# Kernel optimization log

Measured on AMD Instinct MI355X. Metric: run time of the kernel, lower is better.

Reference implementation:

```python
import jax, jax.numpy as jnp
import numpy as np

L, B, S, D = 8, 1, 4096, 2048
H, KVH, HD = 16, 2, 128
Q = 32
THETA = 1e6
MROPE = (16, 24, 24)  # mrope_section, sums to HD//2
EPS = 1e-6


def setup_inputs() -> dict:
    key = jax.random.key(0)
    ks = jax.random.split(key, 8)
    hidden_states = jax.random.normal(ks[0], (L, B, S, D), dtype=jnp.float32)
    ln_w = jax.random.uniform(ks[1], (L, D), dtype=jnp.float32, minval=0.5, maxval=1.5)
    q_w = jax.random.normal(ks[2], (L, D, H * HD), dtype=jnp.float32) * 0.02
    q_b = jax.random.normal(ks[3], (L, H * HD), dtype=jnp.float32) * 0.02
    k_w = jax.random.normal(ks[4], (L, D, KVH * HD), dtype=jnp.float32) * 0.02
    k_b = jax.random.normal(ks[5], (L, KVH * HD), dtype=jnp.float32) * 0.02
    position_ids = jax.random.randint(ks[6], (3, B, S), 0, S, dtype=jnp.int32)
    q_idx = jnp.sort(jax.random.randint(ks[7], (Q,), 0, S, dtype=jnp.int32))
    return {"hidden_states": hidden_states, "ln_w": ln_w, "q_w": q_w, "q_b": q_b,
            "k_w": k_w, "k_b": k_b, "position_ids": position_ids, "q_idx": q_idx}


def _rot_half(x):
    h = x.shape[-1] // 2
    return jnp.concatenate([-x[..., h:], x[..., :h]], axis=-1)


def _mrope_combine(t):
    # t: (3, B, S, HD). Split last dim per 2*mrope_section, chunk i taken from axis i%3.
    parts, off = [], 0
    for i, sec in enumerate(MROPE):
        w = 2 * sec
        parts.append(t[i % 3, :, :, off:off + w])
        off += w
    return jnp.concatenate(parts, axis=-1)[:, None, :, :]  # (B, 1, S, HD)


def reference(hidden_states, ln_w, q_w, q_b, k_w, k_b, position_ids, q_idx):
    # Rotary embeddings from 3D mRoPE position ids
    inv_freq = 1.0 / (THETA ** (jnp.arange(0, HD, 2, dtype=jnp.float32) / HD))  # (HD/2,)
    freqs = position_ids.astype(jnp.float32)[..., None] * inv_freq  # (3, B, S, HD/2)
    emb = jnp.concatenate([freqs, freqs], axis=-1)  # (3, B, S, HD)
    cos = _mrope_combine(jnp.cos(emb))  # (B, 1, S, HD)
    sin = _mrope_combine(jnp.sin(emb))
    cos_q = cos[:, :, q_idx, :]  # (B, 1, Q, HD)
    sin_q = sin[:, :, q_idx, :]
    # Eager causal mask sliced at query rows: (Q, S)
    mask_add = jnp.where(jnp.arange(S)[None, :] > q_idx[:, None], -1e9, 0.0).astype(jnp.float32)

    scale = 1.0 / np.sqrt(HD).astype(np.float32)

    def per_layer(hs, lw, qw, qb, kw, kb):
        # RMSNorm (input_layernorm)
        var = jnp.mean(jnp.square(hs), axis=-1, keepdims=True)
        x = hs * jax.lax.rsqrt(var + EPS) * lw  # (B, S, D)
        xq = x[:, q_idx, :]  # (B, Q, D)
        k = (jnp.einsum('bsd,de->bse', x, kw) + kb).reshape(B, S, KVH, HD).transpose(0, 2, 1, 3)
        q = (jnp.einsum('bqd,de->bqe', xq, qw) + qb).reshape(B, Q, H, HD).transpose(0, 2, 1, 3)
        k = jnp.repeat(k, H // KVH, axis=1)  # repeat_kv -> (B, H, S, HD)
        k = k * cos + _rot_half(k) * sin
        q = q * cos_q + _rot_half(q) * sin_q
        scores = jnp.einsum('bhqd,bhkd->bhqk', q, k) * scale  # (B, H, Q, S)
        scores = scores + mask_add[None, None]
        return jax.nn.softmax(scores.astype(jnp.float32), axis=-1)

    return jax.vmap(per_layer)(hidden_states, ln_w, q_w, q_b, k_w, k_b)  # (L, B, H, Q, S)
```

## Files before the change

kernel.cpp:

```cpp
#include <hip/hip_runtime.h>
#include <hip/hip_bf16.h>
#include <math.h>

#define LYR 8
#define SEQ 4096
#define DIM 2048
#define NH 16
#define HD 128
#define NQ 32
#define NKV 256
#define NQE 2048

typedef __attribute__((ext_vector_type(8))) short short8;
typedef __attribute__((ext_vector_type(4))) float f32x4;

#define WS_IRQ   0
#define WS_ABLOB 256
#define WS_COS   524544
#define WS_SIN   1048832
#define WS_QBUF  1573120
#define WS_PART  2097408
#define WS_W2    4194560
#define WS_KBLOB 8388864
#define WS_QBLOB 16777472

__device__ __forceinline__ short f2bf(float x) {
  __hip_bfloat16 h = __float2bfloat16(x);
  return *(short*)&h;
}
__device__ __forceinline__ float bf2f(short s) {
  unsigned u = ((unsigned)(unsigned short)s) << 16;
  return __uint_as_float(u);
}

#define GLOAD16(srcp, dstp) \
  __builtin_amdgcn_global_load_lds( \
      (const __attribute__((address_space(1))) unsigned int*)(srcp), \
      (__attribute__((address_space(3))) unsigned int*)(dstp), 16, 0, 0)

__global__ __launch_bounds__(256) void prep_kernel(
    const float* __restrict__ ln_w, const float* __restrict__ k_w,
    short* __restrict__ W2) {
  int kb = blockIdx.x, l = blockIdx.y, t = threadIdx.x;
  const float* kwl = k_w + (size_t)l * DIM * NKV;
  const float* lnl = ln_w + l * DIM;
  short* blob = W2 + (size_t)(l * 64 + kb) * 16384;
  #pragma unroll
  for (int i = 0; i < 4; ++i) {
    int p = t + i * 256;
    int fi = p >> 6, lane = p & 63;
    int n = fi * 16 + (lane & 15);
    int k0 = kb * 32 + (lane >> 4) * 8;
    short hi8[8], lo8[8];
    #pragma unroll
    for (int e = 0; e < 8; ++e) {
      float v = lnl[k0 + e] * kwl[(size_t)(k0 + e) * NKV + n];
      short h = f2bf(v);
      hi8[e] = h;
      lo8[e] = f2bf(v - bf2f(h));
    }
    *(short8*)(blob + p * 8) = *(short8*)hi8;
    *(short8*)(blob + 8192 + p * 8) = *(short8*)lo8;
  }
}

__global__ __launch_bounds__(256) void rmsq_kernel(const float* __restrict__ hs,
                                                   const int* __restrict__ q_idx,
                                                   float* __restrict__ irq) {
  int qi = blockIdx.x, l = blockIdx.y, t = threadIdx.x;
  int s = q_idx[qi];
  const float* row = hs + ((size_t)l * SEQ + s) * DIM;
  float4 v0 = *(const float4*)(row + t * 4);
  float4 v1 = *(const float4*)(row + t * 4 + 1024);
  float acc = v0.x*v0.x + v0.y*v0.y + v0.z*v0.z + v0.w*v0.w
            + v1.x*v1.x + v1.y*v1.y + v1.z*v1.z + v1.w*v1.w;
  #pragma unroll
  for (int off = 32; off >= 1; off >>= 1) acc += __shfl_down(acc, off);
  __shared__ float red[4];
  if ((t & 63) == 0) red[t >> 6] = acc;
  __syncthreads();
  if (t == 0) {
    float tot = red[0] + red[1] + red[2] + red[3];
    irq[l * NQ + qi] = rsqrtf(tot / (float)DIM + 1e-6f);
  }
}

__global__ void cossin_kernel(const int* __restrict__ pos_ids,
                              float* __restrict__ cost, float* __restrict__ sint) {
  int idx = blockIdx.x * 256 + threadIdx.x;
  int s = idx >> 7, d = idx & 127;
  int t = (d < 32) ? 0 : (d < 80 ? 1 : 2);
  int j = d & 63;
  double invf = pow(1000000.0, -(double)j / 64.0);
  double ph = (double)pos_ids[t * SEQ + s] * invf;
  cost[idx] = (float)cos(ph);
  sint[idx] = (float)sin(ph);
}

__global__ __launch_bounds__(256) void xqt_kernel(
    const float* __restrict__ hs, const float* __restrict__ ln_w,
    const int* __restrict__ q_idx, const float* __restrict__ irq,
    short* __restrict__ Ablob) {
  __shared__ int qix[32];
  __shared__ float qir[32];
  int l = blockIdx.x, t = threadIdx.x;
  if (t < 32) { qix[t] = q_idx[t]; qir[t] = irq[l * NQ + t]; }
  __syncthreads();
  int lane = t & 63, g4 = t >> 6;
  short* base = Ablob + (size_t)l * 131072;
  int row = lane & 15, kgl = lane >> 4;
  for (int i = 0; i < 64; ++i) {
    int group = g4 * 64 + i;
    int kb = group >> 2, half = (group >> 1) & 1, mf = group & 1;
    int r = row + mf * 16;
    int k0 = kb * 32 + kgl * 8;
    const float* src = hs + ((size_t)l * SEQ + qix[r]) * DIM + k0;
    const float* lnp = ln_w + l * DIM + k0;
    float ir = qir[r];
    float4 v0 = *(const float4*)src;
    float4 v1 = *(const float4*)(src + 4);
    float4 w0 = *(const float4*)lnp;
    float4 w1 = *(const float4*)(lnp + 4);
    float av[8] = {v0.x*w0.x, v0.y*w0.y, v0.z*w0.z, v0.w*w0.w,
                   v1.x*w1.x, v1.y*w1.y, v1.z*w1.z, v1.w*w1.w};
    short o8[8];
    #pragma unroll
    for (int e = 0; e < 8; ++e) {
      float v = av[e] * ir;
      short h = f2bf(v);
      o8[e] = half ? f2bf(v - bf2f(h)) : h;
    }
    *(short8*)(base + group * 512 + lane * 8) = *(short8*)o8;
  }
}

__global__ __launch_bounds__(256) void kgemm_kernel(
    const float* __restrict__ hs, const short* __restrict__ W2,
    const float* __restrict__ k_b, const float* __restrict__ cost,
    const float* __restrict__ sint, short* __restrict__ Kblob) {
  __shared__ __align__(1024) char SM[81920];

  int t = threadIdx.x;
  int fid = blockIdx.x;
  int l = fid & 7, sb = fid >> 3;
  int s0 = sb * 64;
  int lane = t & 63, w = t >> 6;
  int fr = lane & 15, kg = lane >> 4;
  int arow = t >> 2, akg = t & 3;

  const float* hrow = hs + ((size_t)l * SEQ + s0 + arow) * DIM + akg * 8;
  const char* wbase = (const char*)(W2 + (size_t)l * 64 * 16384);

  int amf = arow >> 4;
  int awoff = amf * 1024 + (((akg * 16 + (arow & 15)) * 16) ^ (akg << 5));
  int aroff = (lane * 16) ^ ((lane >> 4) << 5);

  f32x4 acc[4][4];
  #pragma unroll
  for (int mf = 0; mf < 4; ++mf)
    #pragma unroll
    for (int nf = 0; nf < 4; ++nf) acc[mf][nf] = (f32x4){0.f, 0.f, 0.f, 0.f};
  float sq = 0.f;
  float4 rA0, rA1, rB0, rB1;

  {
    #pragma unroll
    for (int c = 0; c < 8; ++c) {
      int chunk = w * 8 + c;
      GLOAD16(wbase + chunk * 1024 + lane * 16, SM + 16384 + chunk * 1024);
    }
    float4 a0 = *(const float4*)(hrow);
    float4 a1 = *(const float4*)(hrow + 4);
    float av[8] = {a0.x, a0.y, a0.z, a0.w, a1.x, a1.y, a1.z, a1.w};
    short hi8[8], lo8[8];
    #pragma unroll
    for (int e = 0; e < 8; ++e) {
      sq += av[e] * av[e];
      short h = f2bf(av[e]);
      hi8[e] = h;
      lo8[e] = f2bf(av[e] - bf2f(h));
    }
    *(short8*)(SM + awoff) = *(short8*)hi8;
    *(short8*)(SM + 4096 + awoff) = *(short8*)lo8;
    rA0 = *(const float4*)(hrow + 32);
    rA1 = *(const float4*)(hrow + 36);
  }
  __syncthreads();

#define KSTEP(KB, C0, C1, N0, N1) do { \
    int buf_ = (KB) & 1; \
    char* asb_ = SM + buf_ * 8192; \
    char* bsb_ = SM + 16384 + buf_ * 32768; \
    if ((KB) < 63) { \
      const char* src_ = wbase + (size_t)((KB) + 1) * 32768; \
      char* dst_ = SM + 16384 + (buf_ ^ 1) * 32768; \
      _Pragma("unroll") \
      for (int c = 0; c < 8; ++c) { \
        int chunk_ = w * 8 + c; \
        GLOAD16(src_ + chunk_ * 1024 + lane * 16, dst_ + chunk_ * 1024); \
      } \
    } \
    if ((KB) < 62) { \
      N0 = *(const float4*)(hrow + ((KB) + 2) * 32); \
      N1 = *(const float4*)(hrow + ((KB) + 2) * 32 + 4); \
    } \
    short8 ah_[4], al_[4]; \
    _Pragma("unroll") \
    for (int mf = 0; mf < 4; ++mf) { \
      ah_[mf] = *(const short8*)(asb_ + mf * 1024 + aroff); \
      al_[mf] = *(const short8*)(asb_ + 4096 + mf * 1024 + aroff); \
    } \
    __builtin_amdgcn_s_setprio(1); \
    _Pragma("unroll") \
    for (int nf = 0; nf < 4; ++nf) { \
      int f_ = w + nf * 4; \
      short8 bh_ = *(const short8*)(bsb_ + f_ * 1024 + lane * 16); \
      short8 bl_ = *(const short8*)(bsb_ + 16384 + f_ * 1024 + lane * 16); \
      _Pragma("unroll") \
      for (int mf = 0; mf < 4; ++mf) { \
        acc[mf][nf] = __builtin_amdgcn_mfma_f32_16x16x32_bf16(ah_[mf], bh_, acc[mf][nf], 0, 0, 0); \
        acc[mf][nf] = __builtin_amdgcn_mfma_f32_16x16x32_bf16(ah_[mf], bl_, acc[mf][nf], 0, 0, 0); \
        acc[mf][nf] = __builtin_amdgcn_mfma_f32_16x16x32_bf16(al_[mf], bh_, acc[mf][nf], 0, 0, 0); \
      } \
    } \
    __builtin_amdgcn_s_setprio(0); \
    if ((KB) < 63) { \
      char* asn_ = SM + (buf_ ^ 1) * 8192; \
      float av_[8] = {C0.x, C0.y, C0.z, C0.w, C1.x, C1.y, C1.z, C1.w}; \
      short hi8_[8], lo8_[8]; \
      _Pragma("unroll") \
      for (int e = 0; e < 8; ++e) { \
        sq += av_[e] * av_[e]; \
        short h_ = f2bf(av_[e]); \
        hi8_[e] = h_; \
        lo8_[e] = f2bf(av_[e] - bf2f(h_)); \
      } \
      *(short8*)(asn_ + awoff) = *(short8*)hi8_; \
      *(short8*)(asn_ + 4096 + awoff) = *(short8*)lo8_; \
    } \
    __syncthreads(); \
  } while (0)

  for (int kb2 = 0; kb2 < 32; ++kb2) {
    KSTEP(2 * kb2, rA0, rA1, rB0, rB1);
    KSTEP(2 * kb2 + 1, rB0, rB1, rA0, rA1);
  }
#undef KSTEP

  sq += __shfl_xor(sq, 1);
  sq += __shfl_xor(sq, 2);
  float* irs = (float*)(SM + 66560);
  if ((t & 3) == 0) irs[arow] = rsqrtf(sq / (float)DIM + 1e-6f);
  __syncthreads();

  float* Kraw = (float*)SM;
  int j = w * 16 + fr;
  float bias0 = k_b[l * NKV + j];
  float bias1 = k_b[l * NKV + j + 64];
  float bias2 = k_b[l * NKV + j + 128];
  float bias3 = k_b[l * NKV + j + 192];
  #pragma unroll
  for (int mf = 0; mf < 4; ++mf) {
    #pragma unroll
    for (int r = 0; r < 4; ++r) {
      int row = mf * 16 + kg * 4 + r;
      int s = s0 + row;
      float ir = irs[row];
      float v0 = acc[mf][0][r] * ir + bias0;
      float v1 = acc[mf][1][r] * ir + bias1;
      float v2 = acc[mf][2][r] * ir + bias2;
      float v3 = acc[mf][3][r] * ir + bias3;
      float cj = cost[s * HD + j], sj = sint[s * HD + j];
      float cj2 = cost[s * HD + j + 64], sj2 = sint[s * HD + j + 64];
      float* kr = Kraw + row * 260;
      kr[j]       = v0 * cj - v1 * sj;
      kr[j + 64]  = v1 * cj2 + v0 * sj2;
      kr[j + 128] = v2 * cj - v3 * sj;
      kr[j + 192] = v3 * cj2 + v2 * sj2;
    }
  }
  __syncthreads();

  int kc = sb >> 1, fb = (sb & 1) * 4;
  #pragma unroll
  for (int i = 0; i < 8; ++i) {
    int c = t + i * 256;
    int lc = c & 63, fl = (c >> 6) & 3, ts = (c >> 8) & 3, kv = c >> 10;
    int key = fl * 16 + (lc & 15);
    int d0 = kv * 128 + ts * 32 + (lc >> 4) * 8;
    float4 x0 = *(const float4*)(Kraw + key * 260 + d0);
    float4 x1 = *(const float4*)(Kraw + key * 260 + d0 + 4);
    float av[8] = {x0.x, x0.y, x0.z, x0.w, x1.x, x1.y, x1.z, x1.w};
    short hi8[8], lo8[8];
    #pragma unroll
    for (int e = 0; e < 8; ++e) {
      short h = f2bf(av[e]);
      hi8[e] = h;
      lo8[e] = f2bf(av[e] - bf2f(h));
    }
    short* bb = Kblob + (size_t)((l * 2 + kv) * 32 + kc) * 32768
              + (size_t)((ts * 2 + 0) * 8 + fb + fl) * 512 + lc * 8;
    *(short8*)bb = *(short8*)hi8;
    *(short8*)(bb + 4096) = *(short8*)lo8;
  }
}

__global__ __launch_bounds__(512) void qgemm_kernel(
    const float* __restrict__ q_w, const short* __restrict__ Ablob,
    float* __restrict__ part) {
  __shared__ __align__(1024) char SM[131072];
  int t = threadIdx.x;
  int nc = blockIdx.x, ks = blockIdx.y, l = blockIdx.z;
  int lane = t & 63, w = t >> 6;
  int fr = lane & 15, kg = lane >> 4;
  const char* abase = (const char*)(Ablob + (size_t)l * 131072 + (size_t)ks * 32768);
  const float* qwl = q_w + (size_t)l * DIM * NQE;

  #pragma unroll
  for (int c = 0; c < 8; ++c) {
    int chunk = w * 8 + c;
    GLOAD16(abase + chunk * 1024 + lane * 16, SM + chunk * 1024);
  }
  #pragma unroll
  for (int c = 0; c < 4; ++c) {
    int r = w * 4 + c;
    GLOAD16((const char*)(qwl + (size_t)(ks * 512 + r) * NQE + nc * 256) + lane * 16,
            SM + 65536 + r * 1024 + lane * 16);
  }
  f32x4 acc[2][2];
  #pragma unroll
  for (int mf = 0; mf < 2; ++mf)
    #pragma unroll
    for (int nf = 0; nf < 2; ++nf) acc[mf][nf] = (f32x4){0.f, 0.f, 0.f, 0.f};
  __syncthreads();

  for (int ts = 0; ts < 16; ++ts) {
    int buf = ts & 1;
    if (ts < 15) {
      #pragma unroll
      for (int c = 0; c < 4; ++c) {
        int r = w * 4 + c;
        GLOAD16((const char*)(qwl + (size_t)(ks * 512 + (ts + 1) * 32 + r) * NQE + nc * 256) + lane * 16,
                SM + 65536 + (buf ^ 1) * 32768 + r * 1024 + lane * 16);
      }
    }
    short8 ah[2], al[2];
    #pragma unroll
    for (int mf = 0; mf < 2; ++mf) {
      ah[mf] = *(const short8*)(SM + ts * 4096 + mf * 1024 + lane * 16);
      al[mf] = *(const short8*)(SM + ts * 4096 + 2048 + mf * 1024 + lane * 16);
    }
    const float* bt = (const float*)(SM + 65536 + buf * 32768);
    #pragma unroll
    for (int nf = 0; nf < 2; ++nf) {
      int c = w * 32 + nf * 16 + fr;
      short bh8[8], bl8[8];
      #pragma unroll
      for (int e = 0; e < 8; ++e) {
        float v = bt[(kg * 8 + e) * 256 + c];
        short h = f2bf(v);
        bh8[e] = h;
        bl8[e] = f2bf(v - bf2f(h));
      }
      short8 bh = *(short8*)bh8, bl = *(short8*)bl8;
      #pragma unroll
      for (int mf = 0; mf < 2; ++mf) {
        acc[mf][nf] = __builtin_amdgcn_mfma_f32_16x16x32_bf16(ah[mf], bh, acc[mf][nf], 0, 0, 0);
        acc[mf][nf] = __builtin_amdgcn_mfma_f32_16x16x32_bf16(ah[mf], bl, acc[mf][nf], 0, 0, 0);
        acc[mf][nf] = __builtin_amdgcn_mfma_f32_16x16x32_bf16(al[mf], bh, acc[mf][nf], 0, 0, 0);
      }
    }
    __syncthreads();
  }

  #pragma unroll
  for (int mf = 0; mf < 2; ++mf) {
    #pragma unroll
    for (int r = 0; r < 4; ++r) {
      int row = mf * 16 + kg * 4 + r;
      float* prow = part + ((size_t)((ks * LYR + l) * NQ + row)) * NQE + nc * 256;
      #pragma unroll
      for (int nf = 0; nf < 2; ++nf) {
        int col = w * 32 + nf * 16 + fr;
        prow[col] = acc[mf][nf][r];
      }
    }
  }
}

__global__ __launch_bounds__(256) void qred_kernel(
    const float* __restrict__ part, const float* __restrict__ q_b,
    float* __restrict__ Qbuf) {
  int idx = blockIdx.x * 256 + threadIdx.x;
  int n = idx & 2047, q = (idx >> 11) & 31, l = idx >> 16;
  float v = q_b[l * NQE + n];
  #pragma unroll
  for (int ks = 0; ks < 4; ++ks)
    v += part[((size_t)((ks * LYR + l) * NQ + q)) * NQE + n];
  Qbuf[((size_t)l * NQ + q) * NQE + n] = v;
}

__global__ __launch_bounds__(256) void qpack_kernel(
    const float* __restrict__ Qbuf, const float* __restrict__ cost,
    const float* __restrict__ sint, const int* __restrict__ q_idx,
    short* __restrict__ Qblob) {
  int kv = blockIdx.x, l = blockIdx.y, t = threadIdx.x;
  short* blob = Qblob + (size_t)(l * 2 + kv) * 65536;
  #pragma unroll
  for (int i = 0; i < 16; ++i) {
    int p = t + i * 256;
    int ts = p >> 10, f = (p >> 6) & 15, lane = p & 63;
    int row = f * 16 + (lane & 15);
    int hh = row >> 5, q = row & 31;
    int h = kv * 8 + hh;
    int d0 = ts * 32 + (lane >> 4) * 8;
    int s = q_idx[q];
    const float* qrow = Qbuf + ((size_t)l * NQ + q) * NQE + h * HD;
    const float* ct = cost + s * HD;
    const float* st = sint + s * HD;
    short hi8[8], lo8[8];
    #pragma unroll
    for (int e = 0; e < 8; ++e) {
      int d = d0 + e;
      float x = qrow[d];
      float xp = qrow[d ^ 64];
      float v = (d < 64) ? (x * ct[d] - xp * st[d]) : (x * ct[d] + xp * st[d]);
      short h2 = f2bf(v);
      hi8[e] = h2;
      lo8[e] = f2bf(v - bf2f(h2));
    }
    *(short8*)(blob + ((ts * 2 + 0) * 16 + f) * 512 + lane * 8) = *(short8*)hi8;
    *(short8*)(blob + ((ts * 2 + 1) * 16 + f) * 512 + lane * 8) = *(short8*)lo8;
  }
}

__global__ __launch_bounds__(512) void scores_kernel(
    const short* __restrict__ Qblob, const short* __restrict__ Kblob,
    const int* __restrict__ q_idx, float* __restrict__ out) {
  __shared__ short Qs[2][16384];
  __shared__ short Ks[2][8192];
  __shared__ int qiv[32];
  int t = threadIdx.x;
  int kc = blockIdx.x, kv = blockIdx.y, l = blockIdx.z;
  int lane = t & 63, w = t >> 6;
  int wm = w >> 1, wn = w & 1;
  if (t < 32) qiv[t] = q_idx[t];
  const char* qsrc = (const char*)(Qblob + (size_t)(l * 2 + kv) * 65536);
  const char* ksrc = (const char*)(Kblob + (size_t)((l * 2 + kv) * 32 + kc) * 32768);
  #pragma unroll
  for (int c = 0; c < 4; ++c) {
    int off = (w * 4 + c) * 1024;
    GLOAD16(qsrc + off + lane * 16, (char*)Qs[0] + off);
  }
  #pragma unroll
  for (int c = 0; c < 2; ++c) {
    int off = (w * 2 + c) * 1024;
    GLOAD16(ksrc + off + lane * 16, (char*)Ks[0] + off);
  }
  f32x4 acc[4][4];
  #pragma unroll
  for (int mf = 0; mf < 4; ++mf)
    #pragma unroll
    for (int nf = 0; nf < 4; ++nf) acc[mf][nf] = (f32x4){0.f, 0.f, 0.f, 0.f};
  __syncthreads();
  for (int ts = 0; ts < 4; ++ts) {
    int buf = ts & 1;
    if (ts < 3) {
      const char* qs = qsrc + (ts + 1) * 32768;
      const char* ks = ksrc + (ts + 1) * 16384;
      #pragma unroll
      for (int c = 0; c < 4; ++c) {
        int off = (w * 4 + c) * 1024;
        GLOAD16(qs + off + lane * 16, (char*)Qs[(ts + 1) & 1] + off);
      }
      #pragma unroll
      for (int c = 0; c < 2; ++c) {
        int off = (w * 2 + c) * 1024;
        GLOAD16(ks + off + lane * 16, (char*)Ks[(ts + 1) & 1] + off);
      }
    }
    short8 ah[4], al[4];
    #pragma unroll
    for (int mf = 0; mf < 4; ++mf) {
      int f = wm * 4 + mf;
      ah[mf] = *(const short8*)(Qs[buf] + f * 512 + lane * 8);
      al[mf] = *(const short8*)(Qs[buf] + 8192 + f * 512 + lane * 8);
    }
    #pragma unroll
    for (int nf = 0; nf < 4; ++nf) {
      int f = wn * 4 + nf;
      short8 bh = *(const short8*)(Ks[buf] + f * 512 + lane * 8);
      short8 bl = *(const short8*)(Ks[buf] + 4096 + f * 512 + lane * 8);
      #pragma unroll
      for (int mf = 0; mf < 4; ++mf) {
        acc[mf][nf] = __builtin_amdgcn_mfma_f32_16x16x32_bf16(ah[mf], bh, acc[mf][nf], 0, 0, 0);
        acc[mf][nf] = __builtin_amdgcn_mfma_f32_16x16x32_bf16(ah[mf], bl, acc[mf][nf], 0, 0, 0);
        acc[mf][nf] = __builtin_amdgcn_mfma_f32_16x16x32_bf16(al[mf], bh, acc[mf][nf], 0, 0, 0);
      }
    }
    __syncthreads();
  }
  const float scale = 0.088388347648318447f;
  #pragma unroll
  for (int mf = 0; mf < 4; ++mf) {
    #pragma unroll
    for (int r = 0; r < 4; ++r) {
      int rr = wm * 64 + mf * 16 + (lane >> 4) * 4 + r;
      int hh = rr >> 5, q = rr & 31;
      int qv = qiv[q];
      float* orow = out + (((size_t)(l * NH + kv * 8 + hh)) * NQ + q) * SEQ;
      #pragma unroll
      for (int nf = 0; nf < 4; ++nf) {
        int key = kc * 128 + (wn * 4 + nf) * 16 + (lane & 15);
        orow[key] = (key > qv) ? -1e9f : acc[mf][nf][r] * scale;
      }
    }
  }
}

__global__ __launch_bounds__(256) void softmax_kernel(float* __restrict__ out) {
  size_t row = blockIdx.x;
  float* p = out + row * SEQ;
  int t = threadIdx.x;
  float4 v[4];
  float mx = -1e30f;
  #pragma unroll
  for (int i = 0; i < 4; ++i) {
    v[i] = *(const float4*)(p + t * 4 + i * 1024);
    mx = fmaxf(mx, fmaxf(fmaxf(v[i].x, v[i].y), fmaxf(v[i].z, v[i].w)));
  }
  #pragma unroll
  for (int off = 32; off >= 1; off >>= 1) mx = fmaxf(mx, __shfl_xor(mx, off));
  __shared__ float red[4];
  if ((t & 63) == 0) red[t >> 6] = mx;
  __syncthreads();
  mx = fmaxf(fmaxf(red[0], red[1]), fmaxf(red[2], red[3]));
  __syncthreads();
  float sum = 0.f;
  #pragma unroll
  for (int i = 0; i < 4; ++i) {
    v[i].x = __expf(v[i].x - mx); v[i].y = __expf(v[i].y - mx);
    v[i].z = __expf(v[i].z - mx); v[i].w = __expf(v[i].w - mx);
    sum += v[i].x + v[i].y + v[i].z + v[i].w;
  }
  #pragma unroll
  for (int off = 32; off >= 1; off >>= 1) sum += __shfl_xor(sum, off);
  if ((t & 63) == 0) red[t >> 6] = sum;
  __syncthreads();
  sum = red[0] + red[1] + red[2] + red[3];
  float inv = 1.f / sum;
  #pragma unroll
  for (int i = 0; i < 4; ++i) {
    v[i].x *= inv; v[i].y *= inv; v[i].z *= inv; v[i].w *= inv;
    *(float4*)(p + t * 4 + i * 1024) = v[i];
  }
}

extern "C" void kernel_launch(void* const* d_in, const int* in_sizes, int n_in,
                              void* d_out, int out_size, void* d_ws, size_t ws_size,
                              hipStream_t stream) {
  const float* hs   = (const float*)d_in[0];
  const float* ln_w = (const float*)d_in[1];
  const float* q_w  = (const float*)d_in[2];
  const float* q_b  = (const float*)d_in[3];
  const float* k_w  = (const float*)d_in[4];
  const float* k_b  = (const float*)d_in[5];
  const int* pos    = (const int*)d_in[6];
  const int* qidx   = (const int*)d_in[7];
  float* out = (float*)d_out;
  float* ws = (float*)d_ws;
  float* irq   = ws + WS_IRQ;
  short* Ablob = (short*)(ws + WS_ABLOB);
  float* cost  = ws + WS_COS;
  float* sint  = ws + WS_SIN;
  float* Qbuf  = ws + WS_QBUF;
  float* part  = ws + WS_PART;
  short* W2    = (short*)(ws + WS_W2);
  short* Kblob = (short*)(ws + WS_KBLOB);
  short* Qblob = (short*)(ws + WS_QBLOB);

  prep_kernel<<<dim3(64, LYR), 256, 0, stream>>>(ln_w, k_w, W2);
  rmsq_kernel<<<dim3(NQ, LYR), 256, 0, stream>>>(hs, qidx, irq);
  cossin_kernel<<<(SEQ * HD) / 256, 256, 0, stream>>>(pos, cost, sint);
  xqt_kernel<<<LYR, 256, 0, stream>>>(hs, ln_w, qidx, irq, Ablob);
  kgemm_kernel<<<512, 256, 0, stream>>>(hs, W2, k_b, cost, sint, Kblob);
  qgemm_kernel<<<dim3(8, 4, LYR), 512, 0, stream>>>(q_w, Ablob, part);
  qred_kernel<<<2048, 256, 0, stream>>>(part, q_b, Qbuf);
  qpack_kernel<<<dim3(2, LYR), 256, 0, stream>>>(Qbuf, cost, sint, qidx, Qblob);
  scores_kernel<<<dim3(32, 2, LYR), 512, 0, stream>>>(Qblob, Kblob, qidx, out);
  softmax_kernel<<<LYR * NH * NQ, 256, 0, stream>>>(out);
}
```

Before: 277.8 us.

## Load K-GEMM B fragments directly into registers instead of staging through LDS

In the K projection GEMM, each wave now loads its own pre-swizzled weight fragments straight from global memory into double-buffered registers, replacing the global_load_lds staging into shared memory. This cuts the LDS footprint from 80KB to about 65KB and removes the LDS reads for B. The barrier is replaced by a custom one that waits only on lgkmcnt, so outstanding global loads are not drained at each step. The cost is more VGPRs for the register double buffer and direct global-load latency exposed per wave.

```diff
diff --git a/kernel.cpp b/kernel.cpp
--- a/kernel.cpp
+++ b/kernel.cpp
@@ -37,6 +37,8 @@
   __builtin_amdgcn_global_load_lds( \
       (const __attribute__((address_space(1))) unsigned int*)(srcp), \
       (__attribute__((address_space(3))) unsigned int*)(dstp), 16, 0, 0)
+
+#define RBAR() asm volatile("s_waitcnt lgkmcnt(0)\n\ts_barrier" ::: "memory")
 
 __global__ __launch_bounds__(256) void prep_kernel(
     const float* __restrict__ ln_w, const float* __restrict__ k_w,
@@ -138,7 +140,7 @@
     const float* __restrict__ hs, const short* __restrict__ W2,
     const float* __restrict__ k_b, const float* __restrict__ cost,
     const float* __restrict__ sint, short* __restrict__ Kblob) {
-  __shared__ __align__(1024) char SM[81920];
+  __shared__ __align__(1024) char SM[67072];
 
   int t = threadIdx.x;
   int fid = blockIdx.x;
@@ -150,6 +152,7 @@
 
   const float* hrow = hs + ((size_t)l * SEQ + s0 + arow) * DIM + akg * 8;
   const char* wbase = (const char*)(W2 + (size_t)l * 64 * 16384);
+  const char* wfrag = wbase + w * 1024 + lane * 16;
 
   int amf = arow >> 4;
   int awoff = amf * 1024 + (((akg * 16 + (arow & 15)) * 16) ^ (akg << 5));
@@ -162,12 +165,13 @@
     for (int nf = 0; nf < 4; ++nf) acc[mf][nf] = (f32x4){0.f, 0.f, 0.f, 0.f};
   float sq = 0.f;
   float4 rA0, rA1, rB0, rB1;
+  short8 B0h[4], B0l[4], B1h[4], B1l[4];
 
   {
     #pragma unroll
-    for (int c = 0; c < 8; ++c) {
-      int chunk = w * 8 + c;
-      GLOAD16(wbase + chunk * 1024 + lane * 16, SM + 16384 + chunk * 1024);
+    for (int nf = 0; nf < 4; ++nf) {
+      B0h[nf] = *(const short8*)(wfrag + nf * 4096);
+      B0l[nf] = *(const short8*)(wfrag + nf * 4096 + 16384);
     }
     float4 a0 = *(const float4*)(hrow);
     float4 a1 = *(const float4*)(hrow + 4);
@@ -185,24 +189,22 @@
     rA0 = *(const float4*)(hrow + 32);
     rA1 = *(const float4*)(hrow + 36);
   }
-  __syncthreads();
-
-#define KSTEP(KB, C0, C1, N0, N1) do { \
+  RBAR();
+
+#define KSTEP(KB, CA0, CA1, NA0, NA1, UBH, UBL, PBH, PBL) do { \
     int buf_ = (KB) & 1; \
     char* asb_ = SM + buf_ * 8192; \
-    char* bsb_ = SM + 16384 + buf_ * 32768; \
     if ((KB) < 63) { \
-      const char* src_ = wbase + (size_t)((KB) + 1) * 32768; \
-      char* dst_ = SM + 16384 + (buf_ ^ 1) * 32768; \
+      const char* bsrc_ = wfrag + (size_t)((KB) + 1) * 32768; \
       _Pragma("unroll") \
-      for (int c = 0; c < 8; ++c) { \
-        int chunk_ = w * 8 + c; \
-        GLOAD16(src_ + chunk_ * 1024 + lane * 16, dst_ + chunk_ * 1024); \
+      for (int nf = 0; nf < 4; ++nf) { \
+        PBH[nf] = *(const short8*)(bsrc_ + nf * 4096); \
+        PBL[nf] = *(const short8*)(bsrc_ + nf * 4096 + 16384); \
       } \
     } \
     if ((KB) < 62) { \
-      N0 = *(const float4*)(hrow + ((KB) + 2) * 32); \
-      N1 = *(const float4*)(hrow + ((KB) + 2) * 32 + 4); \
+      NA0 = *(const float4*)(hrow + ((KB) + 2) * 32); \
+      NA1 = *(const float4*)(hrow + ((KB) + 2) * 32 + 4); \
     } \
     short8 ah_[4], al_[4]; \
     _Pragma("unroll") \
@@ -213,20 +215,17 @@
     __builtin_amdgcn_s_setprio(1); \
     _Pragma("unroll") \
     for (int nf = 0; nf < 4; ++nf) { \
-      int f_ = w + nf * 4; \
-      short8 bh_ = *(const short8*)(bsb_ + f_ * 1024 + lane * 16); \
-      short8 bl_ = *(const short8*)(bsb_ + 16384 + f_ * 1024 + lane * 16); \
       _Pragma("unroll") \
       for (int mf = 0; mf < 4; ++mf) { \
-        acc[mf][nf] = __builtin_amdgcn_mfma_f32_16x16x32_bf16(ah_[mf], bh_, acc[mf][nf], 0, 0, 0); \
-        acc[mf][nf] = __builtin_amdgcn_mfma_f32_16x16x32_bf16(ah_[mf], bl_, acc[mf][nf], 0, 0, 0); \
-        acc[mf][nf] = __builtin_amdgcn_mfma_f32_16x16x32_bf16(al_[mf], bh_, acc[mf][nf], 0, 0, 0); \
+        acc[mf][nf] = __builtin_amdgcn_mfma_f32_16x16x32_bf16(ah_[mf], UBH[nf], acc[mf][nf], 0, 0, 0); \
+        acc[mf][nf] = __builtin_amdgcn_mfma_f32_16x16x32_bf16(ah_[mf], UBL[nf], acc[mf][nf], 0, 0, 0); \
+        acc[mf][nf] = __builtin_amdgcn_mfma_f32_16x16x32_bf16(al_[mf], UBH[nf], acc[mf][nf], 0, 0, 0); \
       } \
     } \
     __builtin_amdgcn_s_setprio(0); \
     if ((KB) < 63) { \
       char* asn_ = SM + (buf_ ^ 1) * 8192; \
-      float av_[8] = {C0.x, C0.y, C0.z, C0.w, C1.x, C1.y, C1.z, C1.w}; \
+      float av_[8] = {CA0.x, CA0.y, CA0.z, CA0.w, CA1.x, CA1.y, CA1.z, CA1.w}; \
       short hi8_[8], lo8_[8]; \
       _Pragma("unroll") \
       for (int e = 0; e < 8; ++e) { \
@@ -238,12 +237,12 @@
       *(short8*)(asn_ + awoff) = *(short8*)hi8_; \
       *(short8*)(asn_ + 4096 + awoff) = *(short8*)lo8_; \
     } \
-    __syncthreads(); \
+    RBAR(); \
   } while (0)
 
   for (int kb2 = 0; kb2 < 32; ++kb2) {
-    KSTEP(2 * kb2, rA0, rA1, rB0, rB1);
-    KSTEP(2 * kb2 + 1, rB0, rB1, rA0, rA1);
+    KSTEP(2 * kb2,     rA0, rA1, rB0, rB1, B0h, B0l, B1h, B1l);
+    KSTEP(2 * kb2 + 1, rB0, rB1, rA0, rA1, B1h, B1l, B0h, B0l);
   }
 #undef KSTEP
 
```

Measured after the change: 279.8 us. No clear change (+0.7%).
